# Performance work log

Hardware: AMD Instinct MI355X
Metric: run time of the kernel (lower is better)

## Reference

```python
import jax, jax.numpy as jnp
import numpy as np

IN_CH = 256
OUT_CH = 256
NUM_HEADS = 4
LOCAL_RADIUS = 2
SCALE = OUT_CH ** 0.5  # torch divides by out_channels**0.5


def setup_inputs() -> dict:
    key = jax.random.key(0)
    ks = jax.random.split(key, 7)
    B, C, H, W = 1, IN_CH, 48, 48
    x = jax.random.normal(ks[0], (B, C, H, W), dtype=jnp.float32)
    s = 0.02
    Wq = jax.random.normal(ks[1], (OUT_CH, IN_CH), dtype=jnp.float32) * s
    Wk = jax.random.normal(ks[2], (OUT_CH, IN_CH), dtype=jnp.float32) * s
    Wv = jax.random.normal(ks[3], (OUT_CH, IN_CH), dtype=jnp.float32) * s
    bq = jax.random.normal(ks[4], (OUT_CH,), dtype=jnp.float32) * s
    bk = jax.random.normal(ks[5], (OUT_CH,), dtype=jnp.float32) * s
    bv = jax.random.normal(ks[6], (OUT_CH,), dtype=jnp.float32) * s
    return {"x": x, "Wq": Wq, "bq": bq, "Wk": Wk, "bk": bk, "Wv": Wv, "bv": bv}


def reference(x, Wq, bq, Wk, bk, Wv, bv):
    B, C, H, W = x.shape
    N = H * W
    # Faithful to torch: x.view(B, N, -1) is a raw reshape of [B,C,H,W]
    xr = x.reshape(B, N, C)
    q = xr @ Wq.T + bq  # [B, N, OUT_CH]
    k = xr @ Wk.T + bk
    v = xr @ Wv.T + bv
    dh = OUT_CH // NUM_HEADS
    # [B, heads, N, dh]
    q = q.reshape(B, N, NUM_HEADS, dh).transpose(0, 2, 1, 3)
    k = k.reshape(B, N, NUM_HEADS, dh).transpose(0, 2, 1, 3)
    v = v.reshape(B, N, NUM_HEADS, dh).transpose(0, 2, 1, 3)
    acc = jnp.zeros_like(v)
    for h in range(-LOCAL_RADIUS, LOCAL_RADIUS + 1):
        for w in range(-LOCAL_RADIUS, LOCAL_RADIUS + 1):
            # torch rolls dims (-3, -2) of [B, heads, N, dh] -> axes (1, 2)
            rk = jnp.roll(k, shift=(h, w), axis=(1, 2))
            scores = jnp.einsum('bhnd,bhmd->bhnm', q, rk) / SCALE
            p = jax.nn.softmax(scores, axis=-1)  # dropout p=0 -> identity
            rv = jnp.roll(v, shift=(-h, -w), axis=(1, 2))
            acc = acc + jnp.einsum('bhnm,bhmd->bhnd', p, rv)
    out = acc.transpose(0, 2, 1, 3).reshape(B, N, NUM_HEADS * dh)
    return out
```

## Files before the change

### kernel.cpp

```cpp
#include <hip/hip_runtime.h>


#define N_TOK 2304
#define OUTC 256
#define HSZ (N_TOK * 64)

typedef _Float16 half8 __attribute__((ext_vector_type(8)));
typedef _Float16 half4 __attribute__((ext_vector_type(4)));
typedef __fp16 fp16x2 __attribute__((ext_vector_type(2)));
typedef float f32x4 __attribute__((ext_vector_type(4)));

typedef __attribute__((address_space(3))) unsigned int as3_u32;
typedef __attribute__((address_space(1))) unsigned int as1_u32;

__device__ __forceinline__ f32x4 mfma16(half8 a, half8 b, f32x4 c) {
  return __builtin_amdgcn_mfma_f32_16x16x32_f16(a, b, c, 0, 0, 0);
}

__device__ __forceinline__ void gload_lds16(const _Float16* g, _Float16* l) {
  __builtin_amdgcn_global_load_lds((const as1_u32*)g, (as3_u32*)l, 16, 0, 0);
}

union H8U { half8 h8; fp16x2 h2[4]; };

__device__ __forceinline__ half8 pack_f32x8(const float* e) {
  H8U u;
  u.h2[0] = __builtin_amdgcn_cvt_pkrtz(e[0], e[1]);
  u.h2[1] = __builtin_amdgcn_cvt_pkrtz(e[2], e[3]);
  u.h2[2] = __builtin_amdgcn_cvt_pkrtz(e[4], e[5]);
  u.h2[3] = __builtin_amdgcn_cvt_pkrtz(e[6], e[7]);
  return u.h8;
}

__global__ __launch_bounds__(256) void k_proj(
    const float* __restrict__ x, const float* __restrict__ Wq,
    const float* __restrict__ Wk, const float* __restrict__ Wv,
    const float* __restrict__ bq, const float* __restrict__ bk,
    const float* __restrict__ bv,
    _Float16* __restrict__ Qh, _Float16* __restrict__ KF, float* __restrict__ VfT) {
  __shared__ _Float16 stg[4096];
  const int w = threadIdx.x >> 6, lane = threadIdx.x & 63;
  const int lr = lane & 15, lk = lane >> 4;
  const int n0 = blockIdx.x * 64 + w * 16;
  const int o0 = blockIdx.y * 64;
  const int mat = blockIdx.z;
  const float* W = (mat == 0) ? Wq : (mat == 1) ? Wk : Wv;
  f32x4 acc[4] = {};
  const float* xrow = x + (size_t)(n0 + lr) * OUTC + 8 * lk;
#pragma unroll
  for (int kk = 0; kk < 8; ++kk) {
    float af[8];
    *(float4*)&af[0] = *(const float4*)(xrow + 32 * kk);
    *(float4*)&af[4] = *(const float4*)(xrow + 32 * kk + 4);
    half8 a = pack_f32x8(af);
#pragma unroll
    for (int c = 0; c < 4; ++c) {
      const float* wrow = W + (size_t)(o0 + 16*c + lr) * OUTC + 32*kk + 8*lk;
      float bf[8];
      *(float4*)&bf[0] = *(const float4*)(wrow);
      *(float4*)&bf[4] = *(const float4*)(wrow + 4);
      half8 b = pack_f32x8(bf);
      acc[c] = mfma16(a, b, acc[c]);
    }
  }
  const float* bias = (mat == 0) ? bq : (mat == 1) ? bk : bv;
  const int hd = blockIdx.y;

  if (mat == 2) {
#pragma unroll
    for (int c = 0; c < 4; ++c) {
      int o = o0 + 16*c + lr;
      float bo = bias[o];
      float4 vv;
      vv.x = acc[c][0] + bo; vv.y = acc[c][1] + bo;
      vv.z = acc[c][2] + bo; vv.w = acc[c][3] + bo;
      *(float4*)(VfT + (size_t)o * N_TOK + n0 + 4*lk) = vv;
    }
    return;
  }

  if (mat == 0) {
    const float qs = 0.0625f * 1.4426950408889634f;
#pragma unroll
    for (int c = 0; c < 4; ++c) {
      float bo = bias[o0 + 16*c + lr];
      int d = 16*c + lr;
#pragma unroll
      for (int r = 0; r < 4; ++r)
        stg[(w*16 + 4*lk + r) * 64 + d] = (_Float16)((acc[c][r] + bo) * qs);
    }
    __syncthreads();
    _Float16* dst = Qh + ((size_t)hd * N_TOK + blockIdx.x * 64) * 64;
    ((half8*)dst)[threadIdx.x]       = ((const half8*)stg)[threadIdx.x];
    ((half8*)dst)[256 + threadIdx.x] = ((const half8*)stg)[256 + threadIdx.x];
  } else {
#pragma unroll
    for (int c = 0; c < 4; ++c) {
      float bo = bias[o0 + 16*c + lr];
      int d = 16*c + lr;
      int h = d >> 5, g4K = (d >> 3) & 3, iiK = d & 7;
#pragma unroll
      for (int r = 0; r < 4; ++r)
        stg[(w*2 + h)*512 + (g4K*16 + 4*lk + r)*8 + iiK] = (_Float16)(acc[c][r] + bo);
    }
    __syncthreads();
    _Float16* dst = KF + (size_t)hd * HSZ + (size_t)blockIdx.x * 4096;
    ((half8*)dst)[threadIdx.x]       = ((const half8*)stg)[threadIdx.x];
    ((half8*)dst)[256 + threadIdx.x] = ((const half8*)stg)[256 + threadIdx.x];
  }
}

__global__ __launch_bounds__(256) void k_smooth(
    const float* __restrict__ VfT, _Float16* __restrict__ VF) {
  __shared__ float Ls[64][76];
  const int t = blockIdx.x, vh = blockIdx.y;
  for (int idx = threadIdx.x; idx < 64 * 72; idx += 256) {
    int rr = idx / 72, cc = idx % 72;
    int j = t*64 - 4 + cc; j = (j + N_TOK) % N_TOK;
    Ls[rr][cc] = VfT[(size_t)(vh*64 + rr) * N_TOK + j];
  }
  __syncthreads();
  for (int f = threadIdx.x; f < 512; f += 256) {
    int cc = f >> 7, h = (f >> 6) & 1, g4 = (f >> 4) & 3, lr = f & 15;
    int row = 16*cc + lr;
    int base = 4 + 32*h + 4*g4;
    half8 out;
#pragma unroll
    for (int i = 0; i < 8; ++i) {
      int loc = base + 16*(i >> 2) + (i & 3);
      float s = Ls[row][loc-4] + Ls[row][loc-2] + Ls[row][loc]
              + Ls[row][loc+2] + Ls[row][loc+4];
      out[i] = (_Float16)s;
    }
    *(half8*)(VF + (size_t)vh * HSZ + (size_t)t * 4096 + f * 8) = out;
  }
}

__global__ __launch_bounds__(256) void k_flash(
    const _Float16* __restrict__ Qh, const _Float16* __restrict__ KF,
    const _Float16* __restrict__ VF,
    _Float16* __restrict__ Opart, float* __restrict__ Lpart) {
  __shared__ __align__(16) _Float16 lds[2][8192];
  const int wv = threadIdx.x >> 6, lane = threadIdx.x & 63;
  const int lr = lane & 15, g4 = lane >> 4;
  const int strip = blockIdx.x * 4 + wv;
  const int n0 = strip * 32;
  const int pair = blockIdx.y;
  const int hd = pair >> 2, gk = pair & 3;
  const int chunk = blockIdx.z;
  const int vh = (2*hd + 4 - gk) & 3;

  const _Float16* Qp = Qh + ((size_t)hd * N_TOK + n0 + lr) * 64 + 8*g4;
  const half8 qa0 = *(const half8*)(Qp);
  const half8 qa1 = *(const half8*)(Qp + 32);
  const half8 qb0 = *(const half8*)(Qp + 16*64);
  const half8 qb1 = *(const half8*)(Qp + 16*64 + 32);

  const _Float16* Kt = KF + (size_t)gk * HSZ + (size_t)chunk * 9 * 4096;
  const _Float16* Vt = VF + (size_t)vh * HSZ + (size_t)chunk * 9 * 4096;
  const _Float16* gsrc = (wv < 2 ? Kt : Vt) + (wv & 1) * 2048 + lane * 8;
  const int ldsoff = (wv < 2 ? 0 : 4096) + (wv & 1) * 2048;

  f32x4 accA[4] = {}, accB[4] = {};
  f32x4 acclA = {}, acclB = {};
  half8 ones;
#pragma unroll
  for (int i = 0; i < 8; ++i) ones[i] = (_Float16)1.0f;

  auto stage = [&](int t, int b) {
    const _Float16* s = gsrc + (size_t)t * 4096;
    _Float16* d = &lds[b][ldsoff];
    gload_lds16(s,        d);
    gload_lds16(s + 512,  d + 512);
    gload_lds16(s + 1024, d + 1024);
    gload_lds16(s + 1536, d + 1536);
  };
  auto body = [&](int b) {
    const _Float16* ldsK = &lds[b][0]    + lane * 8;
    const _Float16* ldsV = &lds[b][4096] + lane * 8;
    f32x4 sA[4], sB[4];
    __builtin_amdgcn_s_setprio(1);
#pragma unroll
    for (int c = 0; c < 4; ++c) {
      half8 k0 = *(const half8*)(ldsK + c*1024);
      half8 k1 = *(const half8*)(ldsK + c*1024 + 512);
      f32x4 tA = {}; tA = mfma16(k0, qa0, tA); tA = mfma16(k1, qa1, tA); sA[c] = tA;
      f32x4 tB = {}; tB = mfma16(k0, qb0, tB); tB = mfma16(k1, qb1, tB); sB[c] = tB;
    }
    __builtin_amdgcn_s_setprio(0);
    H8U a0, a1, b0, b1;
#pragma unroll
    for (int c = 0; c < 4; ++c) {
      float eA0 = __builtin_amdgcn_exp2f(sA[c][0]);
      float eA1 = __builtin_amdgcn_exp2f(sA[c][1]);
      float eA2 = __builtin_amdgcn_exp2f(sA[c][2]);
      float eA3 = __builtin_amdgcn_exp2f(sA[c][3]);
      float eB0 = __builtin_amdgcn_exp2f(sB[c][0]);
      float eB1 = __builtin_amdgcn_exp2f(sB[c][1]);
      float eB2 = __builtin_amdgcn_exp2f(sB[c][2]);
      float eB3 = __builtin_amdgcn_exp2f(sB[c][3]);
      H8U* da = (c < 2) ? &a0 : &a1;
      H8U* db = (c < 2) ? &b0 : &b1;
      int base = (c & 1) * 2;
      da->h2[base]     = __builtin_amdgcn_cvt_pkrtz(eA0, eA1);
      da->h2[base + 1] = __builtin_amdgcn_cvt_pkrtz(eA2, eA3);
      db->h2[base]     = __builtin_amdgcn_cvt_pkrtz(eB0, eB1);
      db->h2[base + 1] = __builtin_amdgcn_cvt_pkrtz(eB2, eB3);
    }
    __builtin_amdgcn_s_setprio(1);
#pragma unroll
    for (int cc = 0; cc < 4; ++cc) {
      half8 v0 = *(const half8*)(ldsV + cc*1024);
      half8 v1 = *(const half8*)(ldsV + cc*1024 + 512);
      accA[cc] = mfma16(v0, a0.h8, accA[cc]); accA[cc] = mfma16(v1, a1.h8, accA[cc]);
      accB[cc] = mfma16(v0, b0.h8, accB[cc]); accB[cc] = mfma16(v1, b1.h8, accB[cc]);
    }
    acclA = mfma16(ones, a0.h8, acclA); acclA = mfma16(ones, a1.h8, acclA);
    acclB = mfma16(ones, b0.h8, acclB); acclB = mfma16(ones, b1.h8, acclB);
    __builtin_amdgcn_s_setprio(0);
  };

  stage(0, 0);
#pragma unroll 1
  for (int t = 0; t < 9; ++t) {
    if (t < 8) {
      stage(t + 1, (t + 1) & 1);
      asm volatile("s_waitcnt vmcnt(4)" ::: "memory");
    } else {
      asm volatile("s_waitcnt vmcnt(0)" ::: "memory");
    }
    __builtin_amdgcn_sched_barrier(0);
    __builtin_amdgcn_s_barrier();
    __builtin_amdgcn_sched_barrier(0);
    body(t & 1);
    if (t < 8) {
      __builtin_amdgcn_sched_barrier(0);
      __builtin_amdgcn_s_barrier();
    }
  }

  float invA = 1.0f / acclA[0];
  float invB = 1.0f / acclB[0];
  _Float16* Oa = Opart + (((size_t)chunk * 16 + pair) * N_TOK + n0 + lr) * 64;
  _Float16* Ob = Oa + 16 * 64;
#pragma unroll
  for (int cc = 0; cc < 4; ++cc) {
    half4 ha, hb;
#pragma unroll
    for (int r = 0; r < 4; ++r) {
      ha[r] = (_Float16)(accA[cc][r] * invA);
      hb[r] = (_Float16)(accB[cc][r] * invB);
    }
    *(half4*)(Oa + 16*cc + 4*g4) = ha;
    *(half4*)(Ob + 16*cc + 4*g4) = hb;
  }
  if (g4 == 0) {
    Lpart[((size_t)chunk * 16 + pair) * N_TOK + n0 + lr] = acclA[0];
    Lpart[((size_t)chunk * 16 + pair) * N_TOK + n0 + 16 + lr] = acclB[0];
  }
}

__global__ __launch_bounds__(256) void k_combine(
    const _Float16* __restrict__ Opart, const float* __restrict__ Lpart,
    float* __restrict__ out) {
  int gid = blockIdx.x * 256 + threadIdx.x;
  int hd = gid / (N_TOK * 8);
  int rem = gid % (N_TOK * 8);
  int n = rem >> 3, db = (rem & 7) * 8;
  float acc[8] = {};
#pragma unroll
  for (int gk = 0; gk < 4; ++gk) {
    float cg = (((hd - gk) & 3) == 2) ? 2.0f : 1.0f;
    int pair = hd * 4 + gk;
    float la[4], lsum = 0.f;
#pragma unroll
    for (int ch = 0; ch < 4; ++ch) {
      la[ch] = Lpart[((size_t)ch * 16 + pair) * N_TOK + n];
      lsum += la[ch];
    }
    float rs = cg / lsum;
#pragma unroll
    for (int ch = 0; ch < 4; ++ch) {
      half8 v = *(const half8*)(Opart + (((size_t)ch * 16 + pair) * N_TOK + n) * 64 + db);
      float w = la[ch] * rs;
#pragma unroll
      for (int i = 0; i < 8; ++i) acc[i] += w * (float)v[i];
    }
  }
  float* dst = out + (size_t)n * OUTC + hd * 64 + db;
  float4 r0, r1;
  r0.x = acc[0]; r0.y = acc[1]; r0.z = acc[2]; r0.w = acc[3];
  r1.x = acc[4]; r1.y = acc[5]; r1.z = acc[6]; r1.w = acc[7];
  *(float4*)(dst)     = r0;
  *(float4*)(dst + 4) = r1;
}

extern "C" void kernel_launch(void* const* d_in, const int* in_sizes, int n_in,
                              void* d_out, int out_size, void* d_ws, size_t ws_size,
                              hipStream_t stream) {
  (void)in_sizes; (void)n_in; (void)out_size; (void)ws_size;
  const float* x  = (const float*)d_in[0];
  const float* Wq = (const float*)d_in[1];
  const float* bq = (const float*)d_in[2];
  const float* Wk = (const float*)d_in[3];
  const float* bk = (const float*)d_in[4];
  const float* Wv = (const float*)d_in[5];
  const float* bv = (const float*)d_in[6];

  char* ws = (char*)d_ws;
  float*    Lp  = (float*)   (ws);
  _Float16* Qh  = (_Float16*)(ws + 1179648);
  _Float16* KF  = (_Float16*)(ws + 2359296);
  float*    VfT = (float*)   (ws + 3538944);
  _Float16* VF  = (_Float16*)(ws + 5898240);
  _Float16* Op  = (_Float16*)(ws + 7077888);
  float* out = (float*)d_out;

  k_proj   <<<dim3(36, 4, 3), dim3(256), 0, stream>>>(x, Wq, Wk, Wv, bq, bk, bv, Qh, KF, VfT);
  k_smooth <<<dim3(36, 4), dim3(256), 0, stream>>>(VfT, VF);
  k_flash  <<<dim3(18, 16, 4), dim3(256), 0, stream>>>(Qh, KF, VF, Op, Lp);
  k_combine<<<dim3(288), dim3(256), 0, stream>>>(Op, Lp, out);
}
```

Before: 67.74 us.

## Fuse V smoothing into projection by pre-summing shifted x rows

The 5-tap smoothing of V along tokens is moved before the linear projection: x rows at offsets -4..4 step 2 are summed, then multiplied by Wv, with the bias scaled by 5. This removes the separate k_smooth kernel launch and the fp32 VfT intermediate round-trip through global memory. In exchange the V projection blocks do five times as many x loads, and summation happens in fp32 before the fp16 conversion, which slightly changes rounding.

```diff
diff --git a/kernel.cpp b/kernel.cpp
--- a/kernel.cpp
+++ b/kernel.cpp
@@ -37,7 +37,7 @@
     const float* __restrict__ Wk, const float* __restrict__ Wv,
     const float* __restrict__ bq, const float* __restrict__ bk,
     const float* __restrict__ bv,
-    _Float16* __restrict__ Qh, _Float16* __restrict__ KF, float* __restrict__ VfT) {
+    _Float16* __restrict__ Qh, _Float16* __restrict__ KF, _Float16* __restrict__ VF) {
   __shared__ _Float16 stg[4096];
   const int w = threadIdx.x >> 6, lane = threadIdx.x & 63;
   const int lr = lane & 15, lk = lane >> 4;
@@ -46,6 +46,51 @@
   const int mat = blockIdx.z;
   const float* W = (mat == 0) ? Wq : (mat == 1) ? Wk : Wv;
   f32x4 acc[4] = {};
+
+  if (mat == 2) {
+    const float* rp[5];
+#pragma unroll
+    for (int u = 0; u < 5; ++u) {
+      int row = n0 + lr + 2*u - 4;
+      row = (row + N_TOK) % N_TOK;
+      rp[u] = x + (size_t)row * OUTC + 8 * lk;
+    }
+#pragma unroll
+    for (int kk = 0; kk < 8; ++kk) {
+      float af[8] = {};
+#pragma unroll
+      for (int u = 0; u < 5; ++u) {
+        float4 p0 = *(const float4*)(rp[u] + 32 * kk);
+        float4 p1 = *(const float4*)(rp[u] + 32 * kk + 4);
+        af[0] += p0.x; af[1] += p0.y; af[2] += p0.z; af[3] += p0.w;
+        af[4] += p1.x; af[5] += p1.y; af[6] += p1.z; af[7] += p1.w;
+      }
+      half8 a = pack_f32x8(af);
+#pragma unroll
+      for (int c = 0; c < 4; ++c) {
+        const float* wrow = W + (size_t)(o0 + 16*c + lr) * OUTC + 32*kk + 8*lk;
+        float bf[8];
+        *(float4*)&bf[0] = *(const float4*)(wrow);
+        *(float4*)&bf[4] = *(const float4*)(wrow + 4);
+        half8 b = pack_f32x8(bf);
+        acc[c] = mfma16(a, b, acc[c]);
+      }
+    }
+#pragma unroll
+    for (int c = 0; c < 4; ++c) {
+      float bo = 5.0f * bv[o0 + 16*c + lr];
+#pragma unroll
+      for (int r = 0; r < 4; ++r)
+        stg[(c*128 + (w>>1)*64 + lk*16 + lr)*8 + 4*(w&1) + r] =
+            (_Float16)(acc[c][r] + bo);
+    }
+    __syncthreads();
+    _Float16* dst = VF + (size_t)blockIdx.y * HSZ + (size_t)blockIdx.x * 4096;
+    ((half8*)dst)[threadIdx.x]       = ((const half8*)stg)[threadIdx.x];
+    ((half8*)dst)[256 + threadIdx.x] = ((const half8*)stg)[256 + threadIdx.x];
+    return;
+  }
+
   const float* xrow = x + (size_t)(n0 + lr) * OUTC + 8 * lk;
 #pragma unroll
   for (int kk = 0; kk < 8; ++kk) {
@@ -63,21 +108,8 @@
       acc[c] = mfma16(a, b, acc[c]);
     }
   }
-  const float* bias = (mat == 0) ? bq : (mat == 1) ? bk : bv;
+  const float* bias = (mat == 0) ? bq : bk;
   const int hd = blockIdx.y;
-
-  if (mat == 2) {
-#pragma unroll
-    for (int c = 0; c < 4; ++c) {
-      int o = o0 + 16*c + lr;
-      float bo = bias[o];
-      float4 vv;
-      vv.x = acc[c][0] + bo; vv.y = acc[c][1] + bo;
-      vv.z = acc[c][2] + bo; vv.w = acc[c][3] + bo;
-      *(float4*)(VfT + (size_t)o * N_TOK + n0 + 4*lk) = vv;
-    }
-    return;
-  }
 
   if (mat == 0) {
     const float qs = 0.0625f * 1.4426950408889634f;
@@ -107,32 +139,6 @@
     _Float16* dst = KF + (size_t)hd * HSZ + (size_t)blockIdx.x * 4096;
     ((half8*)dst)[threadIdx.x]       = ((const half8*)stg)[threadIdx.x];
     ((half8*)dst)[256 + threadIdx.x] = ((const half8*)stg)[256 + threadIdx.x];
-  }
-}
-
-__global__ __launch_bounds__(256) void k_smooth(
-    const float* __restrict__ VfT, _Float16* __restrict__ VF) {
-  __shared__ float Ls[64][76];
-  const int t = blockIdx.x, vh = blockIdx.y;
-  for (int idx = threadIdx.x; idx < 64 * 72; idx += 256) {
-    int rr = idx / 72, cc = idx % 72;
-    int j = t*64 - 4 + cc; j = (j + N_TOK) % N_TOK;
-    Ls[rr][cc] = VfT[(size_t)(vh*64 + rr) * N_TOK + j];
-  }
-  __syncthreads();
-  for (int f = threadIdx.x; f < 512; f += 256) {
-    int cc = f >> 7, h = (f >> 6) & 1, g4 = (f >> 4) & 3, lr = f & 15;
-    int row = 16*cc + lr;
-    int base = 4 + 32*h + 4*g4;
-    half8 out;
-#pragma unroll
-    for (int i = 0; i < 8; ++i) {
-      int loc = base + 16*(i >> 2) + (i & 3);
-      float s = Ls[row][loc-4] + Ls[row][loc-2] + Ls[row][loc]
-              + Ls[row][loc+2] + Ls[row][loc+4];
-      out[i] = (_Float16)s;
-    }
-    *(half8*)(VF + (size_t)vh * HSZ + (size_t)t * 4096 + f * 8) = out;
   }
 }
 
@@ -311,13 +317,11 @@
   float*    Lp  = (float*)   (ws);
   _Float16* Qh  = (_Float16*)(ws + 1179648);
   _Float16* KF  = (_Float16*)(ws + 2359296);
-  float*    VfT = (float*)   (ws + 3538944);
-  _Float16* VF  = (_Float16*)(ws + 5898240);
-  _Float16* Op  = (_Float16*)(ws + 7077888);
+  _Float16* VF  = (_Float16*)(ws + 3538944);
+  _Float16* Op  = (_Float16*)(ws + 4718592);
   float* out = (float*)d_out;
 
-  k_proj   <<<dim3(36, 4, 3), dim3(256), 0, stream>>>(x, Wq, Wk, Wv, bq, bk, bv, Qh, KF, VfT);
-  k_smooth <<<dim3(36, 4), dim3(256), 0, stream>>>(VfT, VF);
+  k_proj   <<<dim3(36, 4, 3), dim3(256), 0, stream>>>(x, Wq, Wk, Wv, bq, bk, bv, Qh, KF, VF);
   k_flash  <<<dim3(18, 16, 4), dim3(256), 0, stream>>>(Qh, KF, VF, Op, Lp);
   k_combine<<<dim3(288), dim3(256), 0, stream>>>(Op, Lp, out);
 }
```

New measurement: 69.22 us. 1.02x slower.
